# Kernel optimization log

Measured on AMD Instinct MI355X. Metric: run time of the kernel, lower is better.

## Reference

```python
import jax, jax.numpy as jnp
import numpy as np


def _soft_proto(x, P):
    d2 = (x * x).sum(-1, keepdims=True) - 2.0 * (x @ P.T) + (P * P).sum(-1)
    w = jax.nn.softmax(-d2, axis=-1)  # scores = -dist_sq, softmax over K
    return w @ P  # soft-matched prototypes


def setup_inputs() -> dict:
    key = jax.random.key(0)
    ks = jax.random.split(key, 12)
    B = 1024
    def u(k, shape, s=0.1):
        return jax.random.uniform(k, shape, minval=-s, maxval=s, dtype=jnp.float32)
    return {
        "fcn": jax.random.normal(ks[0], (B, 90, 90), jnp.float32),
        "scn": jax.random.normal(ks[1], (B, 90, 90), jnp.float32),
        # node embedding Linear(90->48), weights stored [in,out]
        "W_node": u(ks[2], (90, 48)), "b_node": jnp.zeros((48,), jnp.float32),
        "P_node": u(ks[3], (64, 48)),   # node prototypes, init uniform(-0.1,0.1)
        "W_graph": u(ks[4], (48, 32)), "b_graph": jnp.zeros((32,), jnp.float32),
        "P_graph": u(ks[5], (32, 32)),
        "Wg1": u(ks[6], (32, 32)), "bg1": jnp.zeros((32,), jnp.float32),
        "Wg2": u(ks[7], (32, 16)), "bg2": jnp.zeros((16,), jnp.float32),
        "P_cls": u(ks[8], (16, 16)),
        # classifier: final_dim = 2*90*48 + 2*32 + 2*16 = 8736
        "Wc1": u(ks[9], (8736, 256)), "bc1": jnp.zeros((256,), jnp.float32),
        "Wc2": u(ks[10], (256, 3)), "bc2": jnp.zeros((3,), jnp.float32),
    }


def reference(fcn, scn, W_node, b_node, P_node, W_graph, b_graph, P_graph,
              Wg1, bg1, Wg2, bg2, P_cls, Wc1, bc1, Wc2, bc2):
    def branch(x):
        nodes = x @ W_node + b_node                  # [B,90,48]
        nm = _soft_proto(nodes, P_node)              # [B,90,48]
        eg = nm.mean(axis=1) @ W_graph + b_graph     # [B,32]
        gp = _soft_proto(eg, P_graph)                # [B,32]
        ec = jax.nn.relu(gp @ Wg1 + bg1) @ Wg2 + bg2 # [B,16]
        cp = _soft_proto(ec, P_cls)                  # [B,16]
        return nm, gp, cp

    nmf, gpf, cpf = branch(fcn)
    nms, gps, cps = branch(scn)
    B = fcn.shape[0]
    R = jnp.concatenate(
        [nmf.reshape(B, -1), nms.reshape(B, -1), gpf, gps, cpf, cps], axis=-1)  # [B,8736]
    # dropout(0.5) is identity in eval mode
    logits = jax.nn.relu(R @ Wc1 + bc1) @ Wc2 + bc2  # [B,3]
    return logits
```

## Files before the change

### kernel.cpp

```cpp
#include <hip/hip_runtime.h>
#include <hip/hip_bf16.h>

using f16   = _Float16;
using f16x4 = __attribute__((ext_vector_type(4))) _Float16;
using f16x8 = __attribute__((ext_vector_type(8))) _Float16;
using f32x4 = __attribute__((ext_vector_type(4))) float;

__global__ __launch_bounds__(256) void prep_kernel(
    const float* __restrict__ Wn, const float* __restrict__ Pn,
    f16* __restrict__ wf, float* __restrict__ q)
{
  int i = blockIdx.x * 256 + threadIdx.x;
  if (i < 4992) {
    int n = i / 104, k = i - n * 104;
    wf[i] = (k < 90) ? (f16)Wn[k * 48 + n] : (f16)0.f;
  } else if (i < 8576) {
    int j = i - 4992; int p = j / 56, c = j - p * 56;
    wf[i] = (c < 48) ? (f16)Pn[p * 48 + c] : (f16)0.f;
  } else if (i < 12032) {
    int j = i - 8576; int r = j / 72, p = j - r * 72;
    wf[i] = (p < 64) ? (f16)Pn[p * 48 + r] : (f16)0.f;
  } else if (i < 12096) {
    int p = i - 12032;
    float s = 0.f;
    for (int j = 0; j < 48; ++j) { float v = Pn[p * 48 + j]; s = fmaf(v, v, s); }
    q[p] = s;
  }
}

__global__ __launch_bounds__(256) void wc1t_kernel(
    const float* __restrict__ Wc1, f16* __restrict__ Wc1T)
{
  __shared__ f16 sT[32 * 36];
  const int tid = threadIdx.x;
  const int kt = blockIdx.x, ct = blockIdx.y;
  const int c = tid & 31, r4 = (tid >> 5) * 4;
  #pragma unroll
  for (int i = 0; i < 4; ++i) {
    int r = r4 + i;
    sT[c * 36 + r] = (f16)Wc1[(size_t)(kt * 32 + r) * 256 + ct * 32 + c];
  }
  __syncthreads();
  #pragma unroll
  for (int i = 0; i < 4; ++i) {
    int r = r4 + i;
    Wc1T[(size_t)(ct * 32 + r) * 8736 + kt * 32 + c] = sT[r * 36 + c];
  }
}

__global__ __launch_bounds__(256) void node_kernel(
    const float* __restrict__ fcn, const float* __restrict__ scn,
    const float* __restrict__ bn, const f16* __restrict__ wf,
    const float* __restrict__ qg,
    f16* __restrict__ R, float* __restrict__ nmmean)
{
  __shared__ __align__(16) f16 uR[10368];
  __shared__ __align__(16) f16 sWtP[8576];
  __shared__ __align__(16) f16 sNodes[96 * 56];
  __shared__ float sQ[64];
  __shared__ float sMean[96];

  f16* sX   = uR;
  f16* sW   = uR;
  f16* sPnT = uR + 96 * 72;
  f16* sWnT = sWtP;
  f16* sP   = sWtP + 4992;

  const int tid = threadIdx.x;
  const int lane = tid & 63, wv = tid >> 6;
  const int l15 = lane & 15, lg = lane >> 4;
  const int b = blockIdx.x, br = blockIdx.y;

  for (int i = tid; i < 1296; i += 256) ((float4*)uR)[i] = make_float4(0.f, 0.f, 0.f, 0.f);
  for (int i = tid; i < 1072; i += 256) ((f16x8*)sWtP)[i] = ((const f16x8*)wf)[i];
  if (tid < 64) sQ[tid] = qg[tid];
  __syncthreads();

  const float* x = (br ? scn : fcn) + (size_t)b * 8100;
  for (int i = tid; i < 2025; i += 256) {
    float4 v = *(const float4*)&x[i * 4];
    const float vv[4] = {v.x, v.y, v.z, v.w};
    #pragma unroll
    for (int e = 0; e < 4; ++e) {
      int idx = i * 4 + e;
      int r = idx / 90, c = idx - 90 * r;
      sX[r * 104 + c] = (f16)vv[e];
    }
  }
  __syncthreads();

  for (int t = wv; t < 18; t += 4) {
    const int mt = t / 3, nt = t - 3 * mt;
    f32x4 acc = {0.f, 0.f, 0.f, 0.f};
    #pragma unroll
    for (int kt = 0; kt < 3; ++kt) {
      f16x8 a  = *(const f16x8*)&sX[(mt * 16 + l15) * 104 + kt * 32 + lg * 8];
      f16x8 bb = *(const f16x8*)&sWnT[(nt * 16 + l15) * 104 + kt * 32 + lg * 8];
      acc = __builtin_amdgcn_mfma_f32_16x16x32_f16(a, bb, acc, 0, 0, 0);
    }
    const float bias = bn[nt * 16 + l15];
    #pragma unroll
    for (int r = 0; r < 4; ++r)
      sNodes[(mt * 16 + lg * 4 + r) * 56 + nt * 16 + l15] = (f16)(acc[r] + bias);
  }
  __syncthreads();

  for (int mt = wv; mt < 6; mt += 4) {
    f32x4 acc[4];
    #pragma unroll
    for (int nt = 0; nt < 4; ++nt) acc[nt] = (f32x4){0.f, 0.f, 0.f, 0.f};
    const f16x8 a0 = *(const f16x8*)&sNodes[(mt * 16 + l15) * 56 + lg * 8];
    const f16x4 a1 = *(const f16x4*)&sNodes[(mt * 16 + l15) * 56 + 32 + lg * 4];
    #pragma unroll
    for (int nt = 0; nt < 4; ++nt) {
      f16x8 b0 = *(const f16x8*)&sP[(nt * 16 + l15) * 56 + lg * 8];
      acc[nt] = __builtin_amdgcn_mfma_f32_16x16x32_f16(a0, b0, acc[nt], 0, 0, 0);
      f16x4 b1 = *(const f16x4*)&sP[(nt * 16 + l15) * 56 + 32 + lg * 4];
      acc[nt] = __builtin_amdgcn_mfma_f32_16x16x16f16(a1, b1, acc[nt], 0, 0, 0);
    }
    float qv[4];
    #pragma unroll
    for (int nt = 0; nt < 4; ++nt) qv[nt] = sQ[nt * 16 + l15];
    #pragma unroll
    for (int r = 0; r < 4; ++r) {
      float s0 = 2.f * acc[0][r] - qv[0];
      float s1 = 2.f * acc[1][r] - qv[1];
      float s2 = 2.f * acc[2][r] - qv[2];
      float s3 = 2.f * acc[3][r] - qv[3];
      float m = fmaxf(fmaxf(s0, s1), fmaxf(s2, s3));
      m = fmaxf(m, __shfl_xor(m, 1, 64));
      m = fmaxf(m, __shfl_xor(m, 2, 64));
      m = fmaxf(m, __shfl_xor(m, 4, 64));
      m = fmaxf(m, __shfl_xor(m, 8, 64));
      float e0 = __expf(s0 - m), e1 = __expf(s1 - m);
      float e2 = __expf(s2 - m), e3 = __expf(s3 - m);
      float sum = (e0 + e1) + (e2 + e3);
      sum += __shfl_xor(sum, 1, 64);
      sum += __shfl_xor(sum, 2, 64);
      sum += __shfl_xor(sum, 4, 64);
      sum += __shfl_xor(sum, 8, 64);
      const float inv = 1.f / sum;
      const int row = mt * 16 + lg * 4 + r;
      sW[row * 72 + 0 * 16 + l15] = (f16)(e0 * inv);
      sW[row * 72 + 1 * 16 + l15] = (f16)(e1 * inv);
      sW[row * 72 + 2 * 16 + l15] = (f16)(e2 * inv);
      sW[row * 72 + 3 * 16 + l15] = (f16)(e3 * inv);
    }
  }
  for (int i = tid; i < 432; i += 256)
    ((f16x8*)sPnT)[i] = ((const f16x8*)(wf + 8576))[i];
  __syncthreads();

  f16* Rrow = R + (size_t)b * 8736 + (size_t)br * 4320;
  for (int t = wv; t < 18; t += 4) {
    const int mt = t / 3, nt = t - 3 * mt;
    f32x4 acc = {0.f, 0.f, 0.f, 0.f};
    #pragma unroll
    for (int kt = 0; kt < 2; ++kt) {
      f16x8 a  = *(const f16x8*)&sW[(mt * 16 + l15) * 72 + kt * 32 + lg * 8];
      f16x8 bb = *(const f16x8*)&sPnT[(nt * 16 + l15) * 72 + kt * 32 + lg * 8];
      acc = __builtin_amdgcn_mfma_f32_16x16x32_f16(a, bb, acc, 0, 0, 0);
    }
    #pragma unroll
    for (int r = 0; r < 4; ++r) {
      const int row = mt * 16 + lg * 4 + r;
      const f16 hv = (f16)acc[r];
      sNodes[row * 56 + nt * 16 + l15] = hv;
      if (row < 90) Rrow[row * 48 + nt * 16 + l15] = hv;
    }
  }
  __syncthreads();

  if (tid < 96) {
    int j = tid < 48 ? tid : tid - 48;
    int h = tid < 48 ? 0 : 1;
    float s = 0.f;
    for (int i = h * 45; i < h * 45 + 45; ++i) s += (float)sNodes[i * 56 + j];
    sMean[tid] = s;
  }
  __syncthreads();
  if (tid < 48) {
    nmmean[((size_t)br * 1024 + b) * 48 + tid] =
        (sMean[tid] + sMean[48 + tid]) * (1.f / 90.f);
  }
}

__global__ __launch_bounds__(256) void graph_kernel(
    const float* __restrict__ nmmean,
    const float* __restrict__ Wg, const float* __restrict__ bg,
    const float* __restrict__ Pg,
    const float* __restrict__ Wg1, const float* __restrict__ bg1,
    const float* __restrict__ Wg2, const float* __restrict__ bg2,
    const float* __restrict__ Pc,
    f16* __restrict__ R)
{
  __shared__ float sE[4][64];
  __shared__ float sT[4][64];
  const int tid = threadIdx.x;
  const int wid = tid >> 6, lane = tid & 63;
  const int idx = blockIdx.x * 4 + wid;
  const int br = idx >> 10, b = idx & 1023;
  const float* mrow = nmmean + (size_t)idx * 48;
  f16* Rrow = R + (size_t)b * 8736;

  if (lane < 32) {
    float e = bg[lane];
    #pragma unroll
    for (int k = 0; k < 48; ++k) e = fmaf(mrow[k], Wg[k * 32 + lane], e);
    sE[wid][lane] = e;
  }
  __syncthreads();
  if (lane < 32) {
    float s = 0.f;
    #pragma unroll
    for (int j = 0; j < 32; ++j) { float pv = Pg[lane * 32 + j]; s += pv * (2.f * sE[wid][j] - pv); }
    float m = s;
    for (int d = 16; d >= 1; d >>= 1) m = fmaxf(m, __shfl_xor(m, d, 64));
    float ex = __expf(s - m);
    float sum = ex;
    for (int d = 16; d >= 1; d >>= 1) sum += __shfl_xor(sum, d, 64);
    sT[wid][lane] = ex / sum;
  }
  __syncthreads();
  if (lane < 32) {
    float g = 0.f;
    #pragma unroll
    for (int p = 0; p < 32; ++p) g = fmaf(sT[wid][p], Pg[p * 32 + lane], g);
    Rrow[8640 + br * 32 + lane] = (f16)g;
    sE[wid][lane] = g;
  }
  __syncthreads();
  if (lane < 32) {
    float h = bg1[lane];
    #pragma unroll
    for (int k = 0; k < 32; ++k) h = fmaf(sE[wid][k], Wg1[k * 32 + lane], h);
    sT[wid][lane] = fmaxf(h, 0.f);
  }
  __syncthreads();
  if (lane < 16) {
    float c = bg2[lane];
    #pragma unroll
    for (int k = 0; k < 32; ++k) c = fmaf(sT[wid][k], Wg2[k * 16 + lane], c);
    sE[wid][lane] = c;
  }
  __syncthreads();
  if (lane < 16) {
    float s = 0.f;
    #pragma unroll
    for (int j = 0; j < 16; ++j) { float pv = Pc[lane * 16 + j]; s += pv * (2.f * sE[wid][j] - pv); }
    float m = s;
    for (int d = 8; d >= 1; d >>= 1) m = fmaxf(m, __shfl_xor(m, d, 64));
    float ex = __expf(s - m);
    float sum = ex;
    for (int d = 8; d >= 1; d >>= 1) sum += __shfl_xor(sum, d, 64);
    sT[wid][lane] = ex / sum;
  }
  __syncthreads();
  if (lane < 16) {
    float c = 0.f;
    #pragma unroll
    for (int p = 0; p < 16; ++p) c = fmaf(sT[wid][p], Pc[p * 16 + lane], c);
    Rrow[8704 + br * 16 + lane] = (f16)c;
  }
}

__global__ __launch_bounds__(256) void gemm1_kernel(
    const f16* __restrict__ R, const f16* __restrict__ Wc1T,
    float* __restrict__ part, int KS)
{
  __shared__ __align__(16) f16 sA[128 * 40];
  __shared__ __align__(16) f16 sB[64 * 40];
  const int tid = threadIdx.x;
  const int lane = tid & 63, wv = tid >> 6;
  const int l15 = lane & 15, lg = lane >> 4;
  const int wm = wv >> 1, wn = wv & 1;
  const int bm = blockIdx.x * 128, bnc = blockIdx.y * 64, z = blockIdx.z;
  const int base = 273 / KS, rem = 273 - base * KS;
  const int t0 = z * base + (z < rem ? z : rem);
  const int nt_ = base + (z < rem ? 1 : 0);
  const int kbeg = t0 * 32, kend = (t0 + nt_) * 32;

  const int ar = tid >> 1, ah = (tid & 1) * 16;
  const int bc = tid >> 2, bh = (tid & 3) * 8;

  f32x4 acc[4][2];
  #pragma unroll
  for (int mt = 0; mt < 4; ++mt)
    #pragma unroll
    for (int nt = 0; nt < 2; ++nt) acc[mt][nt] = (f32x4){0.f, 0.f, 0.f, 0.f};

  for (int kk = kbeg; kk < kend; kk += 32) {
    const f16* asrc = &R[(size_t)(bm + ar) * 8736 + kk + ah];
    f16x8 v0 = *(const f16x8*)asrc;
    f16x8 v1 = *(const f16x8*)(asrc + 8);
    f16x8 w0 = *(const f16x8*)&Wc1T[(size_t)(bnc + bc) * 8736 + kk + bh];
    *(f16x8*)&sA[ar * 40 + ah] = v0;
    *(f16x8*)&sA[ar * 40 + ah + 8] = v1;
    *(f16x8*)&sB[bc * 40 + bh] = w0;
    __syncthreads();
    #pragma unroll
    for (int mt = 0; mt < 4; ++mt) {
      f16x8 a = *(const f16x8*)&sA[(wm * 64 + mt * 16 + l15) * 40 + lg * 8];
      #pragma unroll
      for (int nt = 0; nt < 2; ++nt) {
        f16x8 bb = *(const f16x8*)&sB[(wn * 32 + nt * 16 + l15) * 40 + lg * 8];
        acc[mt][nt] = __builtin_amdgcn_mfma_f32_16x16x32_f16(a, bb, acc[mt][nt], 0, 0, 0);
      }
    }
    __syncthreads();
  }
  float* pz = part + (size_t)z * 262144;
  #pragma unroll
  for (int mt = 0; mt < 4; ++mt)
    #pragma unroll
    for (int nt = 0; nt < 2; ++nt)
      #pragma unroll
      for (int r = 0; r < 4; ++r)
        pz[(size_t)(bm + wm * 64 + mt * 16 + lg * 4 + r) * 256 +
           bnc + wn * 32 + nt * 16 + l15] = acc[mt][nt][r];
}

__global__ __launch_bounds__(256) void head_kernel(
    const float* __restrict__ part, const float* __restrict__ bc1,
    const float* __restrict__ Wc2, const float* __restrict__ bc2,
    float* __restrict__ out, int KS)
{
  __shared__ float red[3][4];
  const int b = blockIdx.x, t = threadIdx.x;
  float acc = bc1[t];
  for (int z = 0; z < KS; ++z) acc += part[(size_t)z * 262144 + (size_t)b * 256 + t];
  float h = fmaxf(acc, 0.f);
  float p0 = h * Wc2[t * 3 + 0];
  float p1 = h * Wc2[t * 3 + 1];
  float p2 = h * Wc2[t * 3 + 2];
  for (int d = 32; d >= 1; d >>= 1) {
    p0 += __shfl_xor(p0, d, 64);
    p1 += __shfl_xor(p1, d, 64);
    p2 += __shfl_xor(p2, d, 64);
  }
  const int wid = t >> 6, lane = t & 63;
  if (lane == 0) { red[0][wid] = p0; red[1][wid] = p1; red[2][wid] = p2; }
  __syncthreads();
  if (t < 3) {
    out[(size_t)b * 3 + t] = red[t][0] + red[t][1] + red[t][2] + red[t][3] + bc2[t];
  }
}

extern "C" void kernel_launch(void* const* d_in, const int* in_sizes, int n_in,
                              void* d_out, int out_size, void* d_ws, size_t ws_size,
                              hipStream_t stream) {
  const float* fcn     = (const float*)d_in[0];
  const float* scn     = (const float*)d_in[1];
  const float* W_node  = (const float*)d_in[2];
  const float* b_node  = (const float*)d_in[3];
  const float* P_node  = (const float*)d_in[4];
  const float* W_graph = (const float*)d_in[5];
  const float* b_graph = (const float*)d_in[6];
  const float* P_graph = (const float*)d_in[7];
  const float* Wg1     = (const float*)d_in[8];
  const float* bg1     = (const float*)d_in[9];
  const float* Wg2     = (const float*)d_in[10];
  const float* bg2     = (const float*)d_in[11];
  const float* P_cls   = (const float*)d_in[12];
  const float* Wc1     = (const float*)d_in[13];
  const float* bc1     = (const float*)d_in[14];
  const float* Wc2     = (const float*)d_in[15];
  const float* bc2     = (const float*)d_in[16];
  float* out = (float*)d_out;

  char* ws = (char*)d_ws;
  f16*   R16    = (f16*)ws;
  f16*   Wc1T   = (f16*)(ws + 17891328);
  f16*   wf     = (f16*)(ws + 22364160);
  float* qbuf   = (float*)(ws + 22388224);
  float* nmmean = (float*)(ws + 22388480);
  float* part   = (float*)(ws + 22781696);

  size_t avail = ws_size > 22781696u ? ws_size - 22781696u : 0;
  int KS = (int)(avail / 1048576u);
  if (KS > 16) KS = 16;
  if (KS < 1) KS = 1;

  prep_kernel<<<48, 256, 0, stream>>>(W_node, P_node, wf, qbuf);
  wc1t_kernel<<<dim3(273, 8), 256, 0, stream>>>(Wc1, Wc1T);
  node_kernel<<<dim3(1024, 2), 256, 0, stream>>>(fcn, scn, b_node, wf, qbuf,
                                                 R16, nmmean);
  graph_kernel<<<512, 256, 0, stream>>>(nmmean, W_graph, b_graph, P_graph,
                                        Wg1, bg1, Wg2, bg2, P_cls, R16);
  gemm1_kernel<<<dim3(8, 4, KS), 256, 0, stream>>>(R16, Wc1T, part, KS);
  head_kernel<<<1024, 256, 0, stream>>>(part, bc1, Wc2, bc2, out, KS);
}
```

Before: 81.79 us.

## Read node weights from global memory and shrink node_kernel LDS footprint

The node kernel no longer stages the prepared weight and prototype matrices in shared memory. The MFMA B-operands now load directly from the global (cache-resident) prep buffer, and LDS use drops enough to allow a launch bound of 4 blocks per SM. The input tile conversion is rewritten so each thread writes a padded f16x8 row chunk, replacing the separate zeroing pass and the scalar scattered stores, which removes one barrier. The trade-off is that every wave now re-reads weights through L1/L2 instead of from LDS, in exchange for higher occupancy and fewer sync points.

```diff
diff --git a/kernel.cpp b/kernel.cpp
--- a/kernel.cpp
+++ b/kernel.cpp
@@ -48,45 +48,50 @@
   }
 }
 
-__global__ __launch_bounds__(256) void node_kernel(
+__global__ __launch_bounds__(256, 4) void node_kernel(
     const float* __restrict__ fcn, const float* __restrict__ scn,
     const float* __restrict__ bn, const f16* __restrict__ wf,
     const float* __restrict__ qg,
     f16* __restrict__ R, float* __restrict__ nmmean)
 {
-  __shared__ __align__(16) f16 uR[10368];
-  __shared__ __align__(16) f16 sWtP[8576];
+  __shared__ __align__(16) f16 uR[96 * 104];
   __shared__ __align__(16) f16 sNodes[96 * 56];
   __shared__ float sQ[64];
   __shared__ float sMean[96];
 
-  f16* sX   = uR;
-  f16* sW   = uR;
-  f16* sPnT = uR + 96 * 72;
-  f16* sWnT = sWtP;
-  f16* sP   = sWtP + 4992;
+  f16* sX = uR;
+  f16* sW = uR;
+  const f16* Pw   = wf + 4992;
+  const f16* PnTw = wf + 8576;
 
   const int tid = threadIdx.x;
   const int lane = tid & 63, wv = tid >> 6;
   const int l15 = lane & 15, lg = lane >> 4;
   const int b = blockIdx.x, br = blockIdx.y;
 
-  for (int i = tid; i < 1296; i += 256) ((float4*)uR)[i] = make_float4(0.f, 0.f, 0.f, 0.f);
-  for (int i = tid; i < 1072; i += 256) ((f16x8*)sWtP)[i] = ((const f16x8*)wf)[i];
+  const float* x = (br ? scn : fcn) + (size_t)b * 8100;
+  for (int u = tid; u < 1152; u += 256) {
+    const int r = u / 12, c = u - r * 12;
+    f16x8 h;
+    #pragma unroll
+    for (int e = 0; e < 8; ++e) h[e] = (f16)0.f;
+    if (r < 90) {
+      const float* src = x + r * 90 + c * 8;
+      if (c < 11) {
+        float2 a0 = *(const float2*)(src + 0);
+        float2 a1 = *(const float2*)(src + 2);
+        float2 a2 = *(const float2*)(src + 4);
+        float2 a3 = *(const float2*)(src + 6);
+        h[0] = (f16)a0.x; h[1] = (f16)a0.y; h[2] = (f16)a1.x; h[3] = (f16)a1.y;
+        h[4] = (f16)a2.x; h[5] = (f16)a2.y; h[6] = (f16)a3.x; h[7] = (f16)a3.y;
+      } else {
+        float2 a0 = *(const float2*)src;
+        h[0] = (f16)a0.x; h[1] = (f16)a0.y;
+      }
+    }
+    *(f16x8*)&sX[r * 104 + c * 8] = h;
+  }
   if (tid < 64) sQ[tid] = qg[tid];
-  __syncthreads();
-
-  const float* x = (br ? scn : fcn) + (size_t)b * 8100;
-  for (int i = tid; i < 2025; i += 256) {
-    float4 v = *(const float4*)&x[i * 4];
-    const float vv[4] = {v.x, v.y, v.z, v.w};
-    #pragma unroll
-    for (int e = 0; e < 4; ++e) {
-      int idx = i * 4 + e;
-      int r = idx / 90, c = idx - 90 * r;
-      sX[r * 104 + c] = (f16)vv[e];
-    }
-  }
   __syncthreads();
 
   for (int t = wv; t < 18; t += 4) {
@@ -95,7 +100,7 @@
     #pragma unroll
     for (int kt = 0; kt < 3; ++kt) {
       f16x8 a  = *(const f16x8*)&sX[(mt * 16 + l15) * 104 + kt * 32 + lg * 8];
-      f16x8 bb = *(const f16x8*)&sWnT[(nt * 16 + l15) * 104 + kt * 32 + lg * 8];
+      f16x8 bb = *(const f16x8*)&wf[(nt * 16 + l15) * 104 + kt * 32 + lg * 8];
       acc = __builtin_amdgcn_mfma_f32_16x16x32_f16(a, bb, acc, 0, 0, 0);
     }
     const float bias = bn[nt * 16 + l15];
@@ -113,9 +118,9 @@
     const f16x4 a1 = *(const f16x4*)&sNodes[(mt * 16 + l15) * 56 + 32 + lg * 4];
     #pragma unroll
     for (int nt = 0; nt < 4; ++nt) {
-      f16x8 b0 = *(const f16x8*)&sP[(nt * 16 + l15) * 56 + lg * 8];
+      f16x8 b0 = *(const f16x8*)&Pw[(nt * 16 + l15) * 56 + lg * 8];
       acc[nt] = __builtin_amdgcn_mfma_f32_16x16x32_f16(a0, b0, acc[nt], 0, 0, 0);
-      f16x4 b1 = *(const f16x4*)&sP[(nt * 16 + l15) * 56 + 32 + lg * 4];
+      f16x4 b1 = *(const f16x4*)&Pw[(nt * 16 + l15) * 56 + 32 + lg * 4];
       acc[nt] = __builtin_amdgcn_mfma_f32_16x16x16f16(a1, b1, acc[nt], 0, 0, 0);
     }
     float qv[4];
@@ -147,8 +152,6 @@
       sW[row * 72 + 3 * 16 + l15] = (f16)(e3 * inv);
     }
   }
-  for (int i = tid; i < 432; i += 256)
-    ((f16x8*)sPnT)[i] = ((const f16x8*)(wf + 8576))[i];
   __syncthreads();
 
   f16* Rrow = R + (size_t)b * 8736 + (size_t)br * 4320;
@@ -158,7 +161,7 @@
     #pragma unroll
     for (int kt = 0; kt < 2; ++kt) {
       f16x8 a  = *(const f16x8*)&sW[(mt * 16 + l15) * 72 + kt * 32 + lg * 8];
-      f16x8 bb = *(const f16x8*)&sPnT[(nt * 16 + l15) * 72 + kt * 32 + lg * 8];
+      f16x8 bb = *(const f16x8*)&PnTw[(nt * 16 + l15) * 72 + kt * 32 + lg * 8];
       acc = __builtin_amdgcn_mfma_f32_16x16x32_f16(a, bb, acc, 0, 0, 0);
     }
     #pragma unroll
```

Result: faster. 76.16 us (-6.9%).
